# Kernel tuning notes

Measured on AMD Instinct MI355X. Metric: run time of the kernel, lower is better.

## Reference

```python
import jax, jax.numpy as jnp
import numpy as np

N_NODES = 50000
N_EDGES = 600000  # incidence entries; hyperedge ids also live in [0, N_NODES)
HID = 128


def _prelu(x, a):
    return jnp.where(x >= 0, x, a * x)


def _hypergraph_conv(x, W, b, node_idx, edge_idx, num_nodes, num_hedges):
    # PyG HypergraphConv (use_attention=False, heads=1):
    # out = D^{-1} H B^{-1} H^T (X Theta) + bias
    xw = x @ W  # [N, F]
    ones = jnp.ones(node_idx.shape[0], dtype=x.dtype)
    D = jax.ops.segment_sum(ones, node_idx, num_segments=num_nodes)   # node degree
    B = jax.ops.segment_sum(ones, edge_idx, num_segments=num_hedges)  # hyperedge degree
    Dinv = jnp.where(D > 0, 1.0 / D, 0.0)
    Binv = jnp.where(B > 0, 1.0 / B, 0.0)
    # node -> hyperedge aggregation, scaled by B^{-1}
    m = jax.ops.segment_sum(xw[node_idx], edge_idx, num_segments=num_hedges) * Binv[:, None]
    # hyperedge -> node aggregation, scaled by D^{-1}
    out = jax.ops.segment_sum(m[edge_idx], node_idx, num_segments=num_nodes) * Dinv[:, None]
    return out + b


def setup_inputs() -> dict:
    key = jax.random.key(0)
    k1, k2, k3, k4, k5 = jax.random.split(key, 5)
    x = jax.random.normal(k1, (N_NODES, HID), dtype=jnp.float32)
    hyper_edge_index = jax.random.randint(k2, (2, N_EDGES), 0, N_NODES, dtype=jnp.int64)
    # kaiming-normal-ish linear weights, zero biases (per init_weights)
    std = float(np.sqrt(2.0 / HID))
    W1 = jax.random.normal(k3, (HID, HID), dtype=jnp.float32) * std
    W2 = jax.random.normal(k4, (HID, HID), dtype=jnp.float32) * std
    b1 = jnp.zeros((HID,), dtype=jnp.float32)
    b2 = jnp.zeros((HID,), dtype=jnp.float32)
    prelu_a = jnp.full((1,), 0.25, dtype=jnp.float32)  # nn.PReLU default
    return {"x": x, "hyper_edge_index": hyper_edge_index,
            "W1": W1, "b1": b1, "W2": W2, "b2": b2, "prelu_a": prelu_a}


def reference(x, hyper_edge_index, W1, b1, W2, b2, prelu_a):
    node_idx = hyper_edge_index[0]
    edge_idx = hyper_edge_index[1]
    h = _hypergraph_conv(x, W1, b1, node_idx, edge_idx, N_NODES, N_NODES)
    h = _prelu(h, prelu_a)
    h = _hypergraph_conv(h, W2, b2, node_idx, edge_idx, N_NODES, N_NODES)
    h = h + x  # residual
    return _prelu(h, prelu_a)
```

## Files before the change

### kernel.cpp

```cpp
#include <hip/hip_runtime.h>

typedef unsigned short u16;
typedef unsigned int   u32;
typedef unsigned long long u64;

#define HID 128
#define KPB 256
#define NBMAX 512
#define IPB 2048
#define CAP 6144

typedef __bf16 bf16x8 __attribute__((ext_vector_type(8)));
typedef float  f32x4  __attribute__((ext_vector_type(4)));

__device__ inline float u2f(u32 u){ union{u32 u;float f;} v; v.u=u; return v.f; }
__device__ inline u32   f2u(float f){ union{float f;u32 u;} v; v.f=f; return v.u; }
__device__ inline u32  f2bfu(float f){ u32 b=f2u(f); return ((b + 0x7FFFu + ((b>>16)&1u))>>16)&0xFFFFu; }
__device__ inline float blo(u32 u){ return u2f(u<<16); }
__device__ inline float bhi(u32 u){ return u2f(u & 0xFFFF0000u); }
__device__ inline u32  pk(float lo, float hi){ return (f2bfu(hi)<<16) | f2bfu(lo); }

__global__ __launch_bounds__(256) void k_wfrag2(const float* __restrict__ W1, const float* __restrict__ W2,
                                                u16* __restrict__ W1f, u16* __restrict__ W2f,
                                                int* __restrict__ hist, int* __restrict__ bfill,
                                                int* __restrict__ off, int nkeys, int total){
    int gid = blockIdx.x*256 + threadIdx.x;
    if (gid < NBMAX){ hist[gid] = 0; bfill[gid] = 0; }
    if (gid == 0) off[nkeys] = total;
    const float* W = (gid < 16384) ? W1 : W2;
    u16* Wf = (gid < 16384) ? W1f : W2f;
    int id = gid & 16383;
    int i = id & 7, l = (id>>3)&63, j = (id>>9)&7, s = id>>12;
    int k = s*32 + ((l>>4)<<3) + i;
    int n = (j<<4) + (l&15);
    Wf[id] = (u16)f2bfu(W[k*HID + n]);
}

__global__ __launch_bounds__(256) void k_hist(const int* __restrict__ nidx, const int* __restrict__ eidx,
                                              int* __restrict__ hist, int nE, int nN, int nb){
    __shared__ int h[NBMAX];
    for (int t=threadIdx.x; t<nb; t+=256) h[t]=0;
    __syncthreads();
    int base = blockIdx.x*IPB;
    for (int k=threadIdx.x; k<IPB; k+=256){
        int j = base+k;
        if (j < nE){
            int n = nidx[j], e = eidx[j];
            atomicAdd(&h[n>>8], 1);
            atomicAdd(&h[(nN+e)>>8], 1);
        }
    }
    __syncthreads();
    for (int t=threadIdx.x; t<nb; t+=256) if (h[t]) atomicAdd(&hist[t], h[t]);
}

__global__ __launch_bounds__(256) void k_part(const int* __restrict__ nidx, const int* __restrict__ eidx,
                                              const int* __restrict__ hist, int* __restrict__ bfill,
                                              u64* __restrict__ pairs, int nE, int nN, int nb){
    __shared__ int h[NBMAX], rsv[NBMAX], fl[NBMAX], bb[NBMAX], sd[256];
    int t = threadIdx.x;
    for (int i=t; i<nb; i+=256){ h[i]=0; fl[i]=0; }
    __syncthreads();
    int base = blockIdx.x*IPB;
    for (int k=t; k<IPB; k+=256){
        int j = base+k;
        if (j < nE){
            int n = nidx[j], e = eidx[j];
            atomicAdd(&h[n>>8], 1);
            atomicAdd(&h[(nN+e)>>8], 1);
        }
    }
    int c0 = (2*t   < nb) ? hist[2*t]   : 0;
    int c1 = (2*t+1 < nb) ? hist[2*t+1] : 0;
    int s = c0 + c1;
    sd[t] = s; __syncthreads();
    for (int o=1;o<256;o<<=1){ int u = (t>=o)? sd[t-o] : 0; __syncthreads(); sd[t]+=u; __syncthreads(); }
    int ex = sd[t] - s;
    if (2*t   < nb) bb[2*t]   = ex;
    if (2*t+1 < nb) bb[2*t+1] = ex + c0;
    __syncthreads();
    for (int i=t; i<nb; i+=256){ if (h[i]) rsv[i] = bb[i] + atomicAdd(&bfill[i], h[i]); }
    __syncthreads();
    for (int k=t; k<IPB; k+=256){
        int j = base+k;
        if (j < nE){
            int n = nidx[j], e = eidx[j];
            int b1 = n>>8;
            int p1 = rsv[b1] + atomicAdd(&fl[b1], 1);
            pairs[p1] = ((u64)(u32)n << 32) | (u32)e;
            int k2 = nN + e;
            int b2 = k2>>8;
            int p2 = rsv[b2] + atomicAdd(&fl[b2], 1);
            pairs[p2] = ((u64)(u32)k2 << 32) | (u32)n;
        }
    }
}

__global__ __launch_bounds__(256) void k_bucket(const u64* __restrict__ pairs, const int* __restrict__ hist,
                                                int* __restrict__ csr, int* __restrict__ off,
                                                int nkeys, int nb){
    __shared__ int cntS[KPB];
    __shared__ int fillS[KPB];
    __shared__ int bbS[NBMAX+1];
    __shared__ int sd[256];
    __shared__ int vals[CAP];
    int b = blockIdx.x;
    int t = threadIdx.x;
    int c0 = (2*t   < nb) ? hist[2*t]   : 0;
    int c1 = (2*t+1 < nb) ? hist[2*t+1] : 0;
    int s = c0 + c1;
    sd[t] = s; __syncthreads();
    for (int o=1;o<256;o<<=1){ int u = (t>=o)? sd[t-o] : 0; __syncthreads(); sd[t]+=u; __syncthreads(); }
    int ex = sd[t] - s;
    if (2*t   <= nb) bbS[2*t]   = ex;
    if (2*t+1 <= nb) bbS[2*t+1] = ex + c0;
    __syncthreads();
    int base = bbS[b];
    int n = bbS[b+1] - base;
    int k0 = b * KPB;

    cntS[t] = 0;
    __syncthreads();
    for (int i=t; i<n; i+=256){
        u64 p = pairs[base+i];
        int kl = (int)(p>>32) - k0;
        atomicAdd(&cntS[kl], 1);
    }
    __syncthreads();
    int c = cntS[t];
    __syncthreads();
    fillS[t] = c; __syncthreads();
    for (int o=1;o<256;o<<=1){ int u = (t>=o)? fillS[t-o] : 0; __syncthreads(); fillS[t]+=u; __syncthreads(); }
    int ex2 = fillS[t] - c;
    __syncthreads();
    cntS[t] = ex2; fillS[t] = ex2;
    __syncthreads();
    int k = k0 + t;
    if (k < nkeys) off[k] = base + ex2;
    bool fits = (n <= CAP);
    for (int i=t; i<n; i+=256){
        u64 p = pairs[base+i];
        int kl = (int)(p>>32) - k0;
        int pos = atomicAdd(&fillS[kl], 1);
        if (fits) vals[pos] = (int)(u32)p;
        else      csr[base+pos] = (int)(u32)p;
    }
    __syncthreads();
    if (fits){
        for (int i=t; i<n; i+=256) csr[base+i] = vals[i];
    }
}

__global__ __launch_bounds__(256) void k_gemm(const u16* __restrict__ A, const u16* __restrict__ Wf,
                                              u16* __restrict__ C, int M){
    int wave = blockIdx.x*4 + (threadIdx.x>>6);
    int lane = threadIdx.x & 63;
    int rtiles = M >> 4;
    if (wave >= rtiles) return;
    int row0 = wave << 4;

    const u16* Arow = A + (size_t)(row0 + (lane&15))*HID + ((lane>>4)<<3);
    const bf16x8* Wp = reinterpret_cast<const bf16x8*>(Wf) + lane;

    f32x4 acc[8];
    #pragma unroll
    for (int j=0;j<8;++j) acc[j] = (f32x4){0.f,0.f,0.f,0.f};

    #pragma unroll
    for (int s=0;s<4;++s){
        bf16x8 a = *reinterpret_cast<const bf16x8*>(Arow + s*32);
        #pragma unroll
        for (int j=0;j<8;++j){
            bf16x8 b = Wp[(s*8 + j)*64];
            acc[j] = __builtin_amdgcn_mfma_f32_16x16x32_bf16(a, b, acc[j], 0, 0, 0);
        }
    }
    int r0 = row0 + ((lane>>4)<<2);
    int c0 = lane & 15;
    #pragma unroll
    for (int j=0;j<8;++j){
        #pragma unroll
        for (int r=0;r<4;++r){
            C[(size_t)(r0+r)*HID + j*16 + c0] = (u16)f2bfu(acc[j][r]);
        }
    }
}

__global__ __launch_bounds__(256) void k_gemm_f32(const float* __restrict__ A, const u16* __restrict__ Wf,
                                                  u16* __restrict__ C, int M){
    int wave = blockIdx.x*4 + (threadIdx.x>>6);
    int lane = threadIdx.x & 63;
    int rtiles = M >> 4;
    if (wave >= rtiles) return;
    int row0 = wave << 4;

    const float* Arow = A + (size_t)(row0 + (lane&15))*HID + ((lane>>4)<<3);
    const bf16x8* Wp = reinterpret_cast<const bf16x8*>(Wf) + lane;

    f32x4 acc[8];
    #pragma unroll
    for (int j=0;j<8;++j) acc[j] = (f32x4){0.f,0.f,0.f,0.f};

    #pragma unroll
    for (int s=0;s<4;++s){
        float4 f0 = *reinterpret_cast<const float4*>(Arow + s*32);
        float4 f1 = *reinterpret_cast<const float4*>(Arow + s*32 + 4);
        union { u16 h[8]; bf16x8 v; } au;
        au.h[0]=(u16)f2bfu(f0.x); au.h[1]=(u16)f2bfu(f0.y); au.h[2]=(u16)f2bfu(f0.z); au.h[3]=(u16)f2bfu(f0.w);
        au.h[4]=(u16)f2bfu(f1.x); au.h[5]=(u16)f2bfu(f1.y); au.h[6]=(u16)f2bfu(f1.z); au.h[7]=(u16)f2bfu(f1.w);
        #pragma unroll
        for (int j=0;j<8;++j){
            bf16x8 b = Wp[(s*8 + j)*64];
            acc[j] = __builtin_amdgcn_mfma_f32_16x16x32_bf16(au.v, b, acc[j], 0, 0, 0);
        }
    }
    int r0 = row0 + ((lane>>4)<<2);
    int c0 = lane & 15;
    #pragma unroll
    for (int j=0;j<8;++j){
        #pragma unroll
        for (int r=0;r<4;++r){
            C[(size_t)(r0+r)*HID + j*16 + c0] = (u16)f2bfu(acc[j][r]);
        }
    }
}

template<int MODE>
__global__ __launch_bounds__(256) void k_agg(const u32* __restrict__ tab, const int* __restrict__ csr,
                                             const int* __restrict__ off, void* __restrict__ outp,
                                             const float* __restrict__ bias, const float* __restrict__ resid,
                                             const float* __restrict__ aptr, int nrows){
    int d = blockIdx.x*4 + (threadIdx.x>>6);
    if (d >= nrows) return;
    int lane = threadIdx.x & 63;
    int g = lane >> 4;
    int c = lane & 15;
    int start = off[d], end = off[d+1];
    int deg = end - start;

    int myc = 0;
    if (lane < deg) myc = csr[start + lane];

    float a0=0.f,a1=0.f,a2=0.f,a3=0.f,a4=0.f,a5=0.f,a6=0.f,a7=0.f;
    int nb4 = deg < 64 ? deg : 64;
    for (int jb = 0; jb < nb4; jb += 16){
        int j0 = jb + g, j1 = jb + 4 + g, j2 = jb + 8 + g, j3 = jb + 12 + g;
        int s0 = __shfl(myc, j0, 64);
        int s1 = __shfl(myc, j1, 64);
        int s2 = __shfl(myc, j2, 64);
        int s3 = __shfl(myc, j3, 64);
        uint4 v0 = make_uint4(0u,0u,0u,0u), v1 = v0, v2 = v0, v3 = v0;
        if (j0 < nb4) v0 = *reinterpret_cast<const uint4*>(tab + (size_t)s0*64 + (c<<2));
        if (j1 < nb4) v1 = *reinterpret_cast<const uint4*>(tab + (size_t)s1*64 + (c<<2));
        if (j2 < nb4) v2 = *reinterpret_cast<const uint4*>(tab + (size_t)s2*64 + (c<<2));
        if (j3 < nb4) v3 = *reinterpret_cast<const uint4*>(tab + (size_t)s3*64 + (c<<2));
        a0 += blo(v0.x)+blo(v1.x)+blo(v2.x)+blo(v3.x);
        a1 += bhi(v0.x)+bhi(v1.x)+bhi(v2.x)+bhi(v3.x);
        a2 += blo(v0.y)+blo(v1.y)+blo(v2.y)+blo(v3.y);
        a3 += bhi(v0.y)+bhi(v1.y)+bhi(v2.y)+bhi(v3.y);
        a4 += blo(v0.z)+blo(v1.z)+blo(v2.z)+blo(v3.z);
        a5 += bhi(v0.z)+bhi(v1.z)+bhi(v2.z)+bhi(v3.z);
        a6 += blo(v0.w)+blo(v1.w)+blo(v2.w)+blo(v3.w);
        a7 += bhi(v0.w)+bhi(v1.w)+bhi(v2.w)+bhi(v3.w);
    }
    for (int j = start + 64; j < end; ++j){
        uint4 v = make_uint4(0u,0u,0u,0u);
        if (g == 0){
            int src = csr[j];
            v = *reinterpret_cast<const uint4*>(tab + (size_t)src*64 + (c<<2));
        }
        a0 += blo(v.x); a1 += bhi(v.x);
        a2 += blo(v.y); a3 += bhi(v.y);
        a4 += blo(v.z); a5 += bhi(v.z);
        a6 += blo(v.w); a7 += bhi(v.w);
    }
    a0 += __shfl_xor(a0,16,64); a0 += __shfl_xor(a0,32,64);
    a1 += __shfl_xor(a1,16,64); a1 += __shfl_xor(a1,32,64);
    a2 += __shfl_xor(a2,16,64); a2 += __shfl_xor(a2,32,64);
    a3 += __shfl_xor(a3,16,64); a3 += __shfl_xor(a3,32,64);
    a4 += __shfl_xor(a4,16,64); a4 += __shfl_xor(a4,32,64);
    a5 += __shfl_xor(a5,16,64); a5 += __shfl_xor(a5,32,64);
    a6 += __shfl_xor(a6,16,64); a6 += __shfl_xor(a6,32,64);
    a7 += __shfl_xor(a7,16,64); a7 += __shfl_xor(a7,32,64);

    if (g == 0){
        float s = (deg > 0) ? 1.0f/(float)deg : 0.f;
        a0*=s; a1*=s; a2*=s; a3*=s; a4*=s; a5*=s; a6*=s; a7*=s;
        if constexpr (MODE >= 1){
            float4 b0 = *reinterpret_cast<const float4*>(bias + (c<<3));
            float4 b1v = *reinterpret_cast<const float4*>(bias + (c<<3) + 4);
            a0+=b0.x; a1+=b0.y; a2+=b0.z; a3+=b0.w;
            a4+=b1v.x; a5+=b1v.y; a6+=b1v.z; a7+=b1v.w;
        }
        if constexpr (MODE == 2){
            const float* rp = resid + (size_t)d*HID + (c<<3);
            float4 r0 = *reinterpret_cast<const float4*>(rp);
            float4 r1 = *reinterpret_cast<const float4*>(rp + 4);
            a0+=r0.x; a1+=r0.y; a2+=r0.z; a3+=r0.w;
            a4+=r1.x; a5+=r1.y; a6+=r1.z; a7+=r1.w;
        }
        if constexpr (MODE >= 1){
            float al = aptr[0];
            a0 = (a0>=0.f)? a0 : al*a0;  a1 = (a1>=0.f)? a1 : al*a1;
            a2 = (a2>=0.f)? a2 : al*a2;  a3 = (a3>=0.f)? a3 : al*a3;
            a4 = (a4>=0.f)? a4 : al*a4;  a5 = (a5>=0.f)? a5 : al*a5;
            a6 = (a6>=0.f)? a6 : al*a6;  a7 = (a7>=0.f)? a7 : al*a7;
        }
        if constexpr (MODE == 2){
            float* op = (float*)outp + (size_t)d*HID + (c<<3);
            *reinterpret_cast<float4*>(op)     = make_float4(a0,a1,a2,a3);
            *reinterpret_cast<float4*>(op + 4) = make_float4(a4,a5,a6,a7);
        } else {
            uint4 wv;
            wv.x = pk(a0,a1); wv.y = pk(a2,a3); wv.z = pk(a4,a5); wv.w = pk(a6,a7);
            *reinterpret_cast<uint4*>((u32*)outp + (size_t)d*64 + (c<<2)) = wv;
        }
    }
}

extern "C" void kernel_launch(void* const* d_in, const int* in_sizes, int n_in,
                              void* d_out, int out_size, void* d_ws, size_t ws_size,
                              hipStream_t stream){
    (void)n_in; (void)out_size; (void)ws_size;
    const float* x  = (const float*)d_in[0];
    const int*  hei = (const int*)  d_in[1];
    const float* W1 = (const float*)d_in[2];
    const float* b1 = (const float*)d_in[3];
    const float* W2 = (const float*)d_in[4];
    const float* b2 = (const float*)d_in[5];
    const float* ap = (const float*)d_in[6];

    const int nN = in_sizes[0] / HID;
    const int nE = in_sizes[1] / 2;
    const int* nidx = hei;
    const int* eidx = hei + nE;
    const int nkeys = 2*nN;
    const int nb    = (nkeys + KPB - 1) / KPB;

    char* w = (char*)d_ws;
    size_t o = 0;
    auto alloc = [&](size_t bytes)->void*{
        void* p = (void*)(w + o);
        o += (bytes + 255) & ~(size_t)255;
        return p;
    };
    int* hist  = (int*)alloc((size_t)NBMAX*sizeof(int));
    int* bfill = (int*)alloc((size_t)NBMAX*sizeof(int));
    int* off   = (int*)alloc(((size_t)nkeys+1)*sizeof(int));
    int* csr   = (int*)alloc((size_t)2*nE*sizeof(int));
    u64* pairs = (u64*)alloc((size_t)2*nE*sizeof(u64));
    u16* hb    = (u16*)alloc((size_t)nN*HID*sizeof(u16));
    u16* bufB  = (u16*)alloc((size_t)nN*HID*sizeof(u16));
    u16* bufC  = (u16*)alloc((size_t)nN*HID*sizeof(u16));
    u16* w1f   = (u16*)alloc((size_t)HID*HID*sizeof(u16));
    u16* w2f   = (u16*)alloc((size_t)HID*HID*sizeof(u16));

    k_wfrag2<<<128, 256, 0, stream>>>(W1, W2, w1f, w2f, hist, bfill, off, nkeys, 2*nE);

    const int rtiles = nN/16;
    const int ggrid  = (rtiles + 3)/4;
    k_gemm_f32<<<ggrid, 256, 0, stream>>>(x, w1f, bufB, nN);

    const int pgrid = (nE + IPB - 1)/IPB;
    k_hist  <<<pgrid, 256, 0, stream>>>(nidx, eidx, hist, nE, nN, nb);
    k_part  <<<pgrid, 256, 0, stream>>>(nidx, eidx, hist, bfill, pairs, nE, nN, nb);
    k_bucket<<<nb,    256, 0, stream>>>(pairs, hist, csr, off, nkeys, nb);

    const int agrid  = (nN + 3)/4;

    k_agg<0><<<agrid, 256, 0, stream>>>((const u32*)bufB, csr, off + nN, bufC, nullptr, nullptr, nullptr, nN);
    k_agg<1><<<agrid, 256, 0, stream>>>((const u32*)bufC, csr, off,      hb,   b1, nullptr, ap, nN);
    k_gemm<<<ggrid, 256, 0, stream>>>(hb, w2f, bufB, nN);
    k_agg<0><<<agrid, 256, 0, stream>>>((const u32*)bufB, csr, off + nN, bufC, nullptr, nullptr, nullptr, nN);
    k_agg<2><<<agrid, 256, 0, stream>>>((const u32*)bufC, csr, off, d_out, b2, x, ap, nN);
}
```

Measured before the change: 239.8 us.

## Map aggregation rows to 16-lane groups and fuse setup kernels into combined launches

The aggregation kernel now gives each 16-lane group its own destination row, where before a whole 64-lane wave handled one row. It walks the CSR list 16 neighbours at a time with shuffled indices and no longer needs a cross-group shuffle reduction. This is meant to stop wasting lanes, since hyperedges and nodes average only about 12 neighbours. The weight-fragment conversion is folded into the histogram kernel and the first GEMM into the partition kernel as extra blocks, and a memset replaces the in-kernel counter reset, which cuts launch count. One risk is that the CSR index reads can run up to 15 entries past a row's end, which relies on the workspace buffer that follows.

New measurement: 233.5 us. -2.6%, faster.

```diff
diff --git a/kernel.cpp b/kernel.cpp
--- a/kernel.cpp
+++ b/kernel.cpp
@@ -20,85 +20,115 @@
 __device__ inline float bhi(u32 u){ return u2f(u & 0xFFFF0000u); }
 __device__ inline u32  pk(float lo, float hi){ return (f2bfu(hi)<<16) | f2bfu(lo); }
 
-__global__ __launch_bounds__(256) void k_wfrag2(const float* __restrict__ W1, const float* __restrict__ W2,
-                                                u16* __restrict__ W1f, u16* __restrict__ W2f,
-                                                int* __restrict__ hist, int* __restrict__ bfill,
-                                                int* __restrict__ off, int nkeys, int total){
-    int gid = blockIdx.x*256 + threadIdx.x;
-    if (gid < NBMAX){ hist[gid] = 0; bfill[gid] = 0; }
-    if (gid == 0) off[nkeys] = total;
-    const float* W = (gid < 16384) ? W1 : W2;
-    u16* Wf = (gid < 16384) ? W1f : W2f;
-    int id = gid & 16383;
-    int i = id & 7, l = (id>>3)&63, j = (id>>9)&7, s = id>>12;
-    int k = s*32 + ((l>>4)<<3) + i;
-    int n = (j<<4) + (l&15);
-    Wf[id] = (u16)f2bfu(W[k*HID + n]);
-}
-
-__global__ __launch_bounds__(256) void k_hist(const int* __restrict__ nidx, const int* __restrict__ eidx,
-                                              int* __restrict__ hist, int nE, int nN, int nb){
+__global__ __launch_bounds__(256) void k_hist_wfrag(const int* __restrict__ nidx, const int* __restrict__ eidx,
+                                                    int* __restrict__ hist, int nE, int nN, int nb, int nhb,
+                                                    const float* __restrict__ W1, const float* __restrict__ W2,
+                                                    u16* __restrict__ W1f, u16* __restrict__ W2f){
     __shared__ int h[NBMAX];
-    for (int t=threadIdx.x; t<nb; t+=256) h[t]=0;
-    __syncthreads();
-    int base = blockIdx.x*IPB;
-    for (int k=threadIdx.x; k<IPB; k+=256){
-        int j = base+k;
-        if (j < nE){
-            int n = nidx[j], e = eidx[j];
-            atomicAdd(&h[n>>8], 1);
-            atomicAdd(&h[(nN+e)>>8], 1);
-        }
-    }
-    __syncthreads();
-    for (int t=threadIdx.x; t<nb; t+=256) if (h[t]) atomicAdd(&hist[t], h[t]);
-}
-
-__global__ __launch_bounds__(256) void k_part(const int* __restrict__ nidx, const int* __restrict__ eidx,
-                                              const int* __restrict__ hist, int* __restrict__ bfill,
-                                              u64* __restrict__ pairs, int nE, int nN, int nb){
+    if ((int)blockIdx.x < nhb){
+        for (int t=threadIdx.x; t<nb; t+=256) h[t]=0;
+        __syncthreads();
+        int base = blockIdx.x*IPB;
+        for (int k=threadIdx.x; k<IPB; k+=256){
+            int j = base+k;
+            if (j < nE){
+                atomicAdd(&h[nidx[j]>>8], 1);
+                atomicAdd(&h[(nN+eidx[j])>>8], 1);
+            }
+        }
+        __syncthreads();
+        for (int t=threadIdx.x; t<nb; t+=256) if (h[t]) atomicAdd(&hist[t], h[t]);
+    } else {
+        int gid = ((int)blockIdx.x - nhb)*256 + threadIdx.x;
+        const float* W = (gid < 16384) ? W1 : W2;
+        u16* Wf = (gid < 16384) ? W1f : W2f;
+        int id = gid & 16383;
+        int i = id & 7, l = (id>>3)&63, j = (id>>9)&7, s = id>>12;
+        Wf[id] = (u16)f2bfu(W[(s*32 + ((l>>4)<<3) + i)*HID + (j<<4) + (l&15)]);
+    }
+}
+
+__global__ __launch_bounds__(256) void k_part_gemm(const int* __restrict__ nidx, const int* __restrict__ eidx,
+                                                   const int* __restrict__ hist, int* __restrict__ bfill,
+                                                   u64* __restrict__ pairs, int nE, int nN, int nb, int npb,
+                                                   const float* __restrict__ A, const u16* __restrict__ Wf,
+                                                   u16* __restrict__ C, int M){
     __shared__ int h[NBMAX], rsv[NBMAX], fl[NBMAX], bb[NBMAX], sd[256];
     int t = threadIdx.x;
-    for (int i=t; i<nb; i+=256){ h[i]=0; fl[i]=0; }
-    __syncthreads();
-    int base = blockIdx.x*IPB;
-    for (int k=t; k<IPB; k+=256){
-        int j = base+k;
-        if (j < nE){
-            int n = nidx[j], e = eidx[j];
-            atomicAdd(&h[n>>8], 1);
-            atomicAdd(&h[(nN+e)>>8], 1);
-        }
-    }
-    int c0 = (2*t   < nb) ? hist[2*t]   : 0;
-    int c1 = (2*t+1 < nb) ? hist[2*t+1] : 0;
-    int s = c0 + c1;
-    sd[t] = s; __syncthreads();
-    for (int o=1;o<256;o<<=1){ int u = (t>=o)? sd[t-o] : 0; __syncthreads(); sd[t]+=u; __syncthreads(); }
-    int ex = sd[t] - s;
-    if (2*t   < nb) bb[2*t]   = ex;
-    if (2*t+1 < nb) bb[2*t+1] = ex + c0;
-    __syncthreads();
-    for (int i=t; i<nb; i+=256){ if (h[i]) rsv[i] = bb[i] + atomicAdd(&bfill[i], h[i]); }
-    __syncthreads();
-    for (int k=t; k<IPB; k+=256){
-        int j = base+k;
-        if (j < nE){
-            int n = nidx[j], e = eidx[j];
-            int b1 = n>>8;
-            int p1 = rsv[b1] + atomicAdd(&fl[b1], 1);
-            pairs[p1] = ((u64)(u32)n << 32) | (u32)e;
-            int k2 = nN + e;
-            int b2 = k2>>8;
-            int p2 = rsv[b2] + atomicAdd(&fl[b2], 1);
-            pairs[p2] = ((u64)(u32)k2 << 32) | (u32)n;
+    if ((int)blockIdx.x < npb){
+        for (int i=t; i<nb; i+=256){ h[i]=0; fl[i]=0; }
+        __syncthreads();
+        int base = blockIdx.x*IPB;
+        for (int k=t; k<IPB; k+=256){
+            int j = base+k;
+            if (j < nE){
+                atomicAdd(&h[nidx[j]>>8], 1);
+                atomicAdd(&h[(nN+eidx[j])>>8], 1);
+            }
+        }
+        int c0 = (2*t   < nb) ? hist[2*t]   : 0;
+        int c1 = (2*t+1 < nb) ? hist[2*t+1] : 0;
+        int s = c0 + c1;
+        sd[t] = s; __syncthreads();
+        for (int o=1;o<256;o<<=1){ int u = (t>=o)? sd[t-o] : 0; __syncthreads(); sd[t]+=u; __syncthreads(); }
+        int ex = sd[t] - s;
+        if (2*t   < nb) bb[2*t]   = ex;
+        if (2*t+1 < nb) bb[2*t+1] = ex + c0;
+        __syncthreads();
+        for (int i=t; i<nb; i+=256){ if (h[i]) rsv[i] = bb[i] + atomicAdd(&bfill[i], h[i]); }
+        __syncthreads();
+        for (int k=t; k<IPB; k+=256){
+            int j = base+k;
+            if (j < nE){
+                int n = nidx[j], e = eidx[j];
+                int b1 = n>>8;
+                int p1 = rsv[b1] + atomicAdd(&fl[b1], 1);
+                pairs[p1] = ((u64)(u32)n << 32) | (u32)e;
+                int k2 = nN + e;
+                int b2 = k2>>8;
+                int p2 = rsv[b2] + atomicAdd(&fl[b2], 1);
+                pairs[p2] = ((u64)(u32)k2 << 32) | (u32)n;
+            }
+        }
+    } else {
+        int wave = ((int)blockIdx.x - npb)*4 + (t>>6);
+        int lane = t & 63;
+        int rtiles = M >> 4;
+        if (wave >= rtiles) return;
+        int row0 = wave << 4;
+        const float* Arow = A + (size_t)(row0 + (lane&15))*HID + ((lane>>4)<<3);
+        const bf16x8* Wp = reinterpret_cast<const bf16x8*>(Wf) + lane;
+        f32x4 acc[8];
+        #pragma unroll
+        for (int j=0;j<8;++j) acc[j] = (f32x4){0.f,0.f,0.f,0.f};
+        #pragma unroll
+        for (int s=0;s<4;++s){
+            float4 f0 = *reinterpret_cast<const float4*>(Arow + s*32);
+            float4 f1 = *reinterpret_cast<const float4*>(Arow + s*32 + 4);
+            union { u16 h[8]; bf16x8 v; } au;
+            au.h[0]=(u16)f2bfu(f0.x); au.h[1]=(u16)f2bfu(f0.y); au.h[2]=(u16)f2bfu(f0.z); au.h[3]=(u16)f2bfu(f0.w);
+            au.h[4]=(u16)f2bfu(f1.x); au.h[5]=(u16)f2bfu(f1.y); au.h[6]=(u16)f2bfu(f1.z); au.h[7]=(u16)f2bfu(f1.w);
+            #pragma unroll
+            for (int j=0;j<8;++j){
+                bf16x8 b = Wp[(s*8 + j)*64];
+                acc[j] = __builtin_amdgcn_mfma_f32_16x16x32_bf16(au.v, b, acc[j], 0, 0, 0);
+            }
+        }
+        int r0 = row0 + ((lane>>4)<<2);
+        int c0 = lane & 15;
+        #pragma unroll
+        for (int j=0;j<8;++j){
+            #pragma unroll
+            for (int r=0;r<4;++r){
+                C[(size_t)(r0+r)*HID + j*16 + c0] = (u16)f2bfu(acc[j][r]);
+            }
         }
     }
 }
 
 __global__ __launch_bounds__(256) void k_bucket(const u64* __restrict__ pairs, const int* __restrict__ hist,
                                                 int* __restrict__ csr, int* __restrict__ off,
-                                                int nkeys, int nb){
+                                                int nkeys, int nb, int total){
     __shared__ int cntS[KPB];
     __shared__ int fillS[KPB];
     __shared__ int bbS[NBMAX+1];
@@ -106,6 +136,7 @@
     __shared__ int vals[CAP];
     int b = blockIdx.x;
     int t = threadIdx.x;
+    if (b == 0 && t == 0) off[nkeys] = total;
     int c0 = (2*t   < nb) ? hist[2*t]   : 0;
     int c1 = (2*t+1 < nb) ? hist[2*t+1] : 0;
     int s = c0 + c1;
@@ -123,8 +154,7 @@
     __syncthreads();
     for (int i=t; i<n; i+=256){
         u64 p = pairs[base+i];
-        int kl = (int)(p>>32) - k0;
-        atomicAdd(&cntS[kl], 1);
+        atomicAdd(&cntS[(int)(p>>32) - k0], 1);
     }
     __syncthreads();
     int c = cntS[t];
@@ -133,7 +163,7 @@
     for (int o=1;o<256;o<<=1){ int u = (t>=o)? fillS[t-o] : 0; __syncthreads(); fillS[t]+=u; __syncthreads(); }
     int ex2 = fillS[t] - c;
     __syncthreads();
-    cntS[t] = ex2; fillS[t] = ex2;
+    fillS[t] = ex2;
     __syncthreads();
     int k = k0 + t;
     if (k < nkeys) off[k] = base + ex2;
@@ -186,135 +216,74 @@
     }
 }
 
-__global__ __launch_bounds__(256) void k_gemm_f32(const float* __restrict__ A, const u16* __restrict__ Wf,
-                                                  u16* __restrict__ C, int M){
-    int wave = blockIdx.x*4 + (threadIdx.x>>6);
-    int lane = threadIdx.x & 63;
-    int rtiles = M >> 4;
-    if (wave >= rtiles) return;
-    int row0 = wave << 4;
-
-    const float* Arow = A + (size_t)(row0 + (lane&15))*HID + ((lane>>4)<<3);
-    const bf16x8* Wp = reinterpret_cast<const bf16x8*>(Wf) + lane;
-
-    f32x4 acc[8];
-    #pragma unroll
-    for (int j=0;j<8;++j) acc[j] = (f32x4){0.f,0.f,0.f,0.f};
-
-    #pragma unroll
-    for (int s=0;s<4;++s){
-        float4 f0 = *reinterpret_cast<const float4*>(Arow + s*32);
-        float4 f1 = *reinterpret_cast<const float4*>(Arow + s*32 + 4);
-        union { u16 h[8]; bf16x8 v; } au;
-        au.h[0]=(u16)f2bfu(f0.x); au.h[1]=(u16)f2bfu(f0.y); au.h[2]=(u16)f2bfu(f0.z); au.h[3]=(u16)f2bfu(f0.w);
-        au.h[4]=(u16)f2bfu(f1.x); au.h[5]=(u16)f2bfu(f1.y); au.h[6]=(u16)f2bfu(f1.z); au.h[7]=(u16)f2bfu(f1.w);
-        #pragma unroll
-        for (int j=0;j<8;++j){
-            bf16x8 b = Wp[(s*8 + j)*64];
-            acc[j] = __builtin_amdgcn_mfma_f32_16x16x32_bf16(au.v, b, acc[j], 0, 0, 0);
-        }
-    }
-    int r0 = row0 + ((lane>>4)<<2);
-    int c0 = lane & 15;
-    #pragma unroll
-    for (int j=0;j<8;++j){
-        #pragma unroll
-        for (int r=0;r<4;++r){
-            C[(size_t)(r0+r)*HID + j*16 + c0] = (u16)f2bfu(acc[j][r]);
-        }
-    }
-}
-
 template<int MODE>
 __global__ __launch_bounds__(256) void k_agg(const u32* __restrict__ tab, const int* __restrict__ csr,
                                              const int* __restrict__ off, void* __restrict__ outp,
                                              const float* __restrict__ bias, const float* __restrict__ resid,
                                              const float* __restrict__ aptr, int nrows){
-    int d = blockIdx.x*4 + (threadIdx.x>>6);
+    int lane = threadIdx.x & 63;
+    int g = lane >> 4, c = lane & 15;
+    int d = blockIdx.x*16 + ((threadIdx.x>>6)<<2) + g;
     if (d >= nrows) return;
-    int lane = threadIdx.x & 63;
-    int g = lane >> 4;
-    int c = lane & 15;
     int start = off[d], end = off[d+1];
     int deg = end - start;
-
-    int myc = 0;
-    if (lane < deg) myc = csr[start + lane];
+    int gbase = g << 4;
 
     float a0=0.f,a1=0.f,a2=0.f,a3=0.f,a4=0.f,a5=0.f,a6=0.f,a7=0.f;
-    int nb4 = deg < 64 ? deg : 64;
-    for (int jb = 0; jb < nb4; jb += 16){
-        int j0 = jb + g, j1 = jb + 4 + g, j2 = jb + 8 + g, j3 = jb + 12 + g;
-        int s0 = __shfl(myc, j0, 64);
-        int s1 = __shfl(myc, j1, 64);
-        int s2 = __shfl(myc, j2, 64);
-        int s3 = __shfl(myc, j3, 64);
-        uint4 v0 = make_uint4(0u,0u,0u,0u), v1 = v0, v2 = v0, v3 = v0;
-        if (j0 < nb4) v0 = *reinterpret_cast<const uint4*>(tab + (size_t)s0*64 + (c<<2));
-        if (j1 < nb4) v1 = *reinterpret_cast<const uint4*>(tab + (size_t)s1*64 + (c<<2));
-        if (j2 < nb4) v2 = *reinterpret_cast<const uint4*>(tab + (size_t)s2*64 + (c<<2));
-        if (j3 < nb4) v3 = *reinterpret_cast<const uint4*>(tab + (size_t)s3*64 + (c<<2));
-        a0 += blo(v0.x)+blo(v1.x)+blo(v2.x)+blo(v3.x);
-        a1 += bhi(v0.x)+bhi(v1.x)+bhi(v2.x)+bhi(v3.x);
-        a2 += blo(v0.y)+blo(v1.y)+blo(v2.y)+blo(v3.y);
-        a3 += bhi(v0.y)+bhi(v1.y)+bhi(v2.y)+bhi(v3.y);
-        a4 += blo(v0.z)+blo(v1.z)+blo(v2.z)+blo(v3.z);
-        a5 += bhi(v0.z)+bhi(v1.z)+bhi(v2.z)+bhi(v3.z);
-        a6 += blo(v0.w)+blo(v1.w)+blo(v2.w)+blo(v3.w);
-        a7 += bhi(v0.w)+bhi(v1.w)+bhi(v2.w)+bhi(v3.w);
-    }
-    for (int j = start + 64; j < end; ++j){
-        uint4 v = make_uint4(0u,0u,0u,0u);
-        if (g == 0){
-            int src = csr[j];
-            v = *reinterpret_cast<const uint4*>(tab + (size_t)src*64 + (c<<2));
-        }
-        a0 += blo(v.x); a1 += bhi(v.x);
-        a2 += blo(v.y); a3 += bhi(v.y);
-        a4 += blo(v.z); a5 += bhi(v.z);
-        a6 += blo(v.w); a7 += bhi(v.w);
-    }
-    a0 += __shfl_xor(a0,16,64); a0 += __shfl_xor(a0,32,64);
-    a1 += __shfl_xor(a1,16,64); a1 += __shfl_xor(a1,32,64);
-    a2 += __shfl_xor(a2,16,64); a2 += __shfl_xor(a2,32,64);
-    a3 += __shfl_xor(a3,16,64); a3 += __shfl_xor(a3,32,64);
-    a4 += __shfl_xor(a4,16,64); a4 += __shfl_xor(a4,32,64);
-    a5 += __shfl_xor(a5,16,64); a5 += __shfl_xor(a5,32,64);
-    a6 += __shfl_xor(a6,16,64); a6 += __shfl_xor(a6,32,64);
-    a7 += __shfl_xor(a7,16,64); a7 += __shfl_xor(a7,32,64);
-
-    if (g == 0){
-        float s = (deg > 0) ? 1.0f/(float)deg : 0.f;
-        a0*=s; a1*=s; a2*=s; a3*=s; a4*=s; a5*=s; a6*=s; a7*=s;
-        if constexpr (MODE >= 1){
-            float4 b0 = *reinterpret_cast<const float4*>(bias + (c<<3));
-            float4 b1v = *reinterpret_cast<const float4*>(bias + (c<<3) + 4);
-            a0+=b0.x; a1+=b0.y; a2+=b0.z; a3+=b0.w;
-            a4+=b1v.x; a5+=b1v.y; a6+=b1v.z; a7+=b1v.w;
-        }
-        if constexpr (MODE == 2){
-            const float* rp = resid + (size_t)d*HID + (c<<3);
-            float4 r0 = *reinterpret_cast<const float4*>(rp);
-            float4 r1 = *reinterpret_cast<const float4*>(rp + 4);
-            a0+=r0.x; a1+=r0.y; a2+=r0.z; a3+=r0.w;
-            a4+=r1.x; a5+=r1.y; a6+=r1.z; a7+=r1.w;
-        }
-        if constexpr (MODE >= 1){
-            float al = aptr[0];
-            a0 = (a0>=0.f)? a0 : al*a0;  a1 = (a1>=0.f)? a1 : al*a1;
-            a2 = (a2>=0.f)? a2 : al*a2;  a3 = (a3>=0.f)? a3 : al*a3;
-            a4 = (a4>=0.f)? a4 : al*a4;  a5 = (a5>=0.f)? a5 : al*a5;
-            a6 = (a6>=0.f)? a6 : al*a6;  a7 = (a7>=0.f)? a7 : al*a7;
-        }
-        if constexpr (MODE == 2){
-            float* op = (float*)outp + (size_t)d*HID + (c<<3);
-            *reinterpret_cast<float4*>(op)     = make_float4(a0,a1,a2,a3);
-            *reinterpret_cast<float4*>(op + 4) = make_float4(a4,a5,a6,a7);
-        } else {
-            uint4 wv;
-            wv.x = pk(a0,a1); wv.y = pk(a2,a3); wv.z = pk(a4,a5); wv.w = pk(a6,a7);
-            *reinterpret_cast<uint4*>((u32*)outp + (size_t)d*64 + (c<<2)) = wv;
-        }
+    for (int pos = start; pos < end; pos += 16){
+        int myc = csr[pos + c];
+        int lim = end - pos;
+        #pragma unroll
+        for (int i=0;i<16;i+=4){
+            int s0 = __shfl(myc, gbase|i,     64);
+            int s1 = __shfl(myc, gbase|(i+1), 64);
+            int s2 = __shfl(myc, gbase|(i+2), 64);
+            int s3 = __shfl(myc, gbase|(i+3), 64);
+            uint4 v0 = make_uint4(0u,0u,0u,0u), v1 = v0, v2 = v0, v3 = v0;
+            if (i   < lim) v0 = *reinterpret_cast<const uint4*>(tab + (size_t)s0*64 + (c<<2));
+            if (i+1 < lim) v1 = *reinterpret_cast<const uint4*>(tab + (size_t)s1*64 + (c<<2));
+            if (i+2 < lim) v2 = *reinterpret_cast<const uint4*>(tab + (size_t)s2*64 + (c<<2));
+            if (i+3 < lim) v3 = *reinterpret_cast<const uint4*>(tab + (size_t)s3*64 + (c<<2));
+            a0 += blo(v0.x)+blo(v1.x)+blo(v2.x)+blo(v3.x);
+            a1 += bhi(v0.x)+bhi(v1.x)+bhi(v2.x)+bhi(v3.x);
+            a2 += blo(v0.y)+blo(v1.y)+blo(v2.y)+blo(v3.y);
+            a3 += bhi(v0.y)+bhi(v1.y)+bhi(v2.y)+bhi(v3.y);
+            a4 += blo(v0.z)+blo(v1.z)+blo(v2.z)+blo(v3.z);
+            a5 += bhi(v0.z)+bhi(v1.z)+bhi(v2.z)+bhi(v3.z);
+            a6 += blo(v0.w)+blo(v1.w)+blo(v2.w)+blo(v3.w);
+            a7 += bhi(v0.w)+bhi(v1.w)+bhi(v2.w)+bhi(v3.w);
+        }
+    }
+    float s = (deg > 0) ? 1.0f/(float)deg : 0.f;
+    a0*=s; a1*=s; a2*=s; a3*=s; a4*=s; a5*=s; a6*=s; a7*=s;
+    if constexpr (MODE >= 1){
+        float4 b0 = *reinterpret_cast<const float4*>(bias + (c<<3));
+        float4 b1v = *reinterpret_cast<const float4*>(bias + (c<<3) + 4);
+        a0+=b0.x; a1+=b0.y; a2+=b0.z; a3+=b0.w;
+        a4+=b1v.x; a5+=b1v.y; a6+=b1v.z; a7+=b1v.w;
+    }
+    if constexpr (MODE == 2){
+        const float* rp = resid + (size_t)d*HID + (c<<3);
+        float4 r0 = *reinterpret_cast<const float4*>(rp);
+        float4 r1 = *reinterpret_cast<const float4*>(rp + 4);
+        a0+=r0.x; a1+=r0.y; a2+=r0.z; a3+=r0.w;
+        a4+=r1.x; a5+=r1.y; a6+=r1.z; a7+=r1.w;
+    }
+    if constexpr (MODE >= 1){
+        float al = aptr[0];
+        a0 = (a0>=0.f)? a0 : al*a0;  a1 = (a1>=0.f)? a1 : al*a1;
+        a2 = (a2>=0.f)? a2 : al*a2;  a3 = (a3>=0.f)? a3 : al*a3;
+        a4 = (a4>=0.f)? a4 : al*a4;  a5 = (a5>=0.f)? a5 : al*a5;
+        a6 = (a6>=0.f)? a6 : al*a6;  a7 = (a7>=0.f)? a7 : al*a7;
+    }
+    if constexpr (MODE == 2){
+        float* op = (float*)outp + (size_t)d*HID + (c<<3);
+        *reinterpret_cast<float4*>(op)     = make_float4(a0,a1,a2,a3);
+        *reinterpret_cast<float4*>(op + 4) = make_float4(a4,a5,a6,a7);
+    } else {
+        uint4 wv;
+        wv.x = pk(a0,a1); wv.y = pk(a2,a3); wv.z = pk(a4,a5); wv.w = pk(a6,a7);
+        *reinterpret_cast<uint4*>((u32*)outp + (size_t)d*64 + (c<<2)) = wv;
     }
 }
 
@@ -355,18 +324,18 @@
     u16* w1f   = (u16*)alloc((size_t)HID*HID*sizeof(u16));
     u16* w2f   = (u16*)alloc((size_t)HID*HID*sizeof(u16));
 
-    k_wfrag2<<<128, 256, 0, stream>>>(W1, W2, w1f, w2f, hist, bfill, off, nkeys, 2*nE);
-
+    hipMemsetAsync(hist, 0, (size_t)2*NBMAX*sizeof(int), stream);
+
+    const int pgrid  = (nE + IPB - 1)/IPB;
     const int rtiles = nN/16;
     const int ggrid  = (rtiles + 3)/4;
-    k_gemm_f32<<<ggrid, 256, 0, stream>>>(x, w1f, bufB, nN);
-
-    const int pgrid = (nE + IPB - 1)/IPB;
-    k_hist  <<<pgrid, 256, 0, stream>>>(nidx, eidx, hist, nE, nN, nb);
-    k_part  <<<pgrid, 256, 0, stream>>>(nidx, eidx, hist, bfill, pairs, nE, nN, nb);
-    k_bucket<<<nb,    256, 0, stream>>>(pairs, hist, csr, off, nkeys, nb);
-
-    const int agrid  = (nN + 3)/4;
+
+    k_hist_wfrag<<<pgrid + 128, 256, 0, stream>>>(nidx, eidx, hist, nE, nN, nb, pgrid, W1, W2, w1f, w2f);
+    k_part_gemm<<<pgrid + ggrid, 256, 0, stream>>>(nidx, eidx, hist, bfill, pairs, nE, nN, nb, pgrid,
+                                                   x, w1f, bufB, nN);
+    k_bucket<<<nb, 256, 0, stream>>>(pairs, hist, csr, off, nkeys, nb, 2*nE);
+
+    const int agrid = (nN + 15)/16;
 
     k_agg<0><<<agrid, 256, 0, stream>>>((const u32*)bufB, csr, off + nN, bufC, nullptr, nullptr, nullptr, nN);
     k_agg<1><<<agrid, 256, 0, stream>>>((const u32*)bufC, csr, off,      hb,   b1, nullptr, ap, nN);
```
